# Optimization experiments

Hardware: AMD Instinct MI355X
Metric: run time of the kernel (lower is better)

The kernel has to match this reference:

```python
import jax, jax.numpy as jnp
import numpy as np

IN_F, OUT_F = 4096, 11008
B, S = 2, 4096


def setup_inputs() -> dict:
    key = jax.random.key(0)
    k1, k2, k3, k4 = jax.random.split(key, 4)
    x = jax.random.normal(k1, (B, S, IN_F), dtype=jnp.float32) * 3.0  # pre-smoothed activations
    # int8 weight, stored as int8 (spec'd int32 for harness; math identical)
    weight = jax.random.randint(k2, (OUT_F, IN_F), -127, 128, dtype=jnp.int32).astype(jnp.int8)
    bias = jax.random.normal(k3, (OUT_F,), dtype=jnp.float32)
    dequant_scale = jax.random.uniform(k4, (1,), dtype=jnp.float32) * 0.01 + 0.001  # weight absmax scale
    return {"x": x, "weight": weight, "bias": bias, "dequant_scale": dequant_scale}


def reference(x, weight, bias, dequant_scale):
    x_shape = x.shape
    x2 = x.reshape(-1, x_shape[-1])  # [T, in]
    # per-token activation quantization: absmax -> scale -> round/clamp to int8
    quant_scale = (jnp.max(jnp.abs(x2), axis=-1, keepdims=True) / 127.0).astype(jnp.float32)  # [T,1]
    x_q = jnp.clip(jnp.round(x2 / quant_scale), -128, 127).astype(jnp.int8)
    out_i32 = jnp.matmul(x_q.astype(jnp.int32), weight.astype(jnp.int32).T)  # [T, out]
    # dequant epilogue + bias (all fp32)
    dscale = dequant_scale.reshape(()) * quant_scale  # [T,1]
    out = dscale * out_i32.astype(jnp.float32) + bias
    return out.reshape(*x_shape[:-1], -1).astype(x.dtype)
```

## Files before the change

kernel.cpp:

```cpp
#include <hip/hip_runtime.h>

#define T_TOKENS 8192
#define IN_F 4096
#define OUT_F 11008

#define BM 256
#define BN 256
#define BK 64
#define NT (IN_F / BK)

typedef __attribute__((ext_vector_type(4))) int v4i;
typedef __attribute__((ext_vector_type(16))) int v16i;

__device__ __forceinline__ void load_lds16(const signed char* g, const signed char* l) {
    __builtin_amdgcn_global_load_lds(
        (const __attribute__((address_space(1))) void*)g,
        (__attribute__((address_space(3))) void*)l, 16, 0, 0);
}

__global__ __launch_bounds__(256) void quant_kernel(
        const float* __restrict__ x, signed char* __restrict__ xq,
        float* __restrict__ qscale) {
    const int row = blockIdx.x;
    const float4* xr = (const float4*)(x + (size_t)row * IN_F);
    float4 v[4];
    float am = 0.f;
#pragma unroll
    for (int i = 0; i < 4; ++i) {
        v[i] = xr[threadIdx.x + i * 256];
        am = fmaxf(am, fmaxf(fmaxf(fabsf(v[i].x), fabsf(v[i].y)),
                             fmaxf(fabsf(v[i].z), fabsf(v[i].w))));
    }
#pragma unroll
    for (int off = 32; off > 0; off >>= 1)
        am = fmaxf(am, __shfl_xor(am, off, 64));
    __shared__ float wmax[4];
    const int wid = threadIdx.x >> 6;
    if ((threadIdx.x & 63) == 0) wmax[wid] = am;
    __syncthreads();
    float amax = fmaxf(fmaxf(wmax[0], wmax[1]), fmaxf(wmax[2], wmax[3]));
    float qs = amax * (1.0f / 127.0f);
    if (qs < 1e-30f) qs = 1e-30f;
    const float inv = 1.0f / qs;
    if (threadIdx.x == 0) qscale[row] = qs;
    int* xqo = (int*)(xq + (size_t)row * IN_F);
#pragma unroll
    for (int i = 0; i < 4; ++i) {
        int q0 = (int)rintf(v[i].x * inv);
        int q1 = (int)rintf(v[i].y * inv);
        int q2 = (int)rintf(v[i].z * inv);
        int q3 = (int)rintf(v[i].w * inv);
        q0 = max(-128, min(127, q0));
        q1 = max(-128, min(127, q1));
        q2 = max(-128, min(127, q2));
        q3 = max(-128, min(127, q3));
        unsigned p = (unsigned)(q0 & 255) | ((unsigned)(q1 & 255) << 8) |
                     ((unsigned)(q2 & 255) << 16) | ((unsigned)(q3 & 255) << 24);
        xqo[threadIdx.x + i * 256] = (int)p;
    }
}

__global__ __launch_bounds__(256) void repack_kernel(
        const int* __restrict__ w32, signed char* __restrict__ w8, int n4) {
    int idx = blockIdx.x * 256 + threadIdx.x;
    const int stride = gridDim.x * 256;
    for (int i = idx; i < n4; i += stride) {
        v4i w = ((const v4i*)w32)[i];
        unsigned p = (unsigned)(w[0] & 255) | ((unsigned)(w[1] & 255) << 8) |
                     ((unsigned)(w[2] & 255) << 16) | ((unsigned)(w[3] & 255) << 24);
        ((int*)w8)[i] = (int)p;
    }
}

__global__ __launch_bounds__(512, 2) void gemm_kernel(
        const signed char* __restrict__ A, const signed char* __restrict__ B,
        const float* __restrict__ qscale, const float* __restrict__ bias,
        const float* __restrict__ dqs, float* __restrict__ out) {
    __shared__ __align__(16) signed char smem[3 * 32768];

    const int tid = threadIdx.x;
    const int wid = tid >> 6;
    const int lane = tid & 63;
    const int wm = wid >> 2;
    const int wn = wid & 3;
    const int l31 = lane & 31;
    const int hi = lane >> 5;

    const int b = (int)blockIdx.x;
    const int xcd = b & 7;
    const int idx = b >> 3;
    const int m0 = (xcd * 4 + (idx & 3)) * BM;
    const int n0 = (idx >> 2) * BN;

    const signed char* gSrc[4];
    int ldsOff[4];
#pragma unroll
    for (int c = 0; c < 4; ++c) {
        const int cc = c & 1;
        const int L = cc * 8192 + tid * 16;
        const int row = L >> 6;
        const int slot = (L >> 4) & 3;
        const int col = ((slot ^ ((row >> 1) & 3)) << 4);
        if (c < 2) {
            gSrc[c] = A + (size_t)(m0 + row) * IN_F + col;
            ldsOff[c] = cc * 8192 + wid * 1024;
        } else {
            gSrc[c] = B + (size_t)(n0 + row) * IN_F + col;
            ldsOff[c] = 16384 + cc * 8192 + wid * 1024;
        }
    }

    int aOff[4][2], bOff[2][2];
#pragma unroll
    for (int im = 0; im < 4; ++im) {
        const int r = wm * 128 + im * 32 + l31;
#pragma unroll
        for (int ks = 0; ks < 2; ++ks) {
            const int slot = ks * 2 + hi;
            aOff[im][ks] = r * 64 + ((slot ^ ((r >> 1) & 3)) << 4);
        }
    }
#pragma unroll
    for (int in = 0; in < 2; ++in) {
        const int r = wn * 64 + in * 32 + l31;
#pragma unroll
        for (int ks = 0; ks < 2; ++ks) {
            const int slot = ks * 2 + hi;
            bOff[in][ks] = 16384 + r * 64 + ((slot ^ ((r >> 1) & 3)) << 4);
        }
    }

    v16i acc[4][2] = {};

    int bb0 = 0, bb1 = 32768, bb2 = 65536;
#pragma unroll
    for (int c = 0; c < 4; ++c) load_lds16(gSrc[c], smem + bb0 + ldsOff[c]);
#pragma unroll
    for (int c = 0; c < 4; ++c) load_lds16(gSrc[c] + BK, smem + bb1 + ldsOff[c]);
    asm volatile("s_waitcnt vmcnt(4)" ::: "memory");
    __builtin_amdgcn_sched_barrier(0);
    __builtin_amdgcn_s_barrier();

    for (int t = 0; t < NT; ++t) {
        const int koff2 = (t + 2) * BK;
        const bool stage = (t + 2 < NT);
        v4i a01[2][2], a23[2][2], b0[2], b1[2];

#pragma unroll
        for (int im = 0; im < 2; ++im)
#pragma unroll
            for (int ks = 0; ks < 2; ++ks)
                a01[im][ks] = *(const v4i*)(smem + bb0 + aOff[im][ks]);
#pragma unroll
        for (int ks = 0; ks < 2; ++ks)
            b0[ks] = *(const v4i*)(smem + bb0 + bOff[0][ks]);
        if (stage) load_lds16(gSrc[0] + koff2, smem + bb2 + ldsOff[0]);
        __builtin_amdgcn_sched_barrier(0);
        __builtin_amdgcn_s_barrier();
        asm volatile("s_waitcnt lgkmcnt(0)" ::: "memory");
        __builtin_amdgcn_sched_barrier(0);
        __builtin_amdgcn_s_setprio(1);
#pragma unroll
        for (int ks = 0; ks < 2; ++ks)
#pragma unroll
            for (int im = 0; im < 2; ++im)
                acc[im][0] = __builtin_amdgcn_mfma_i32_32x32x32_i8(
                    a01[im][ks], b0[ks], acc[im][0], 0, 0, 0);
        __builtin_amdgcn_s_setprio(0);
        __builtin_amdgcn_sched_barrier(0);
        __builtin_amdgcn_s_barrier();

#pragma unroll
        for (int ks = 0; ks < 2; ++ks)
            b1[ks] = *(const v4i*)(smem + bb0 + bOff[1][ks]);
        if (stage) load_lds16(gSrc[1] + koff2, smem + bb2 + ldsOff[1]);
        __builtin_amdgcn_sched_barrier(0);
        __builtin_amdgcn_s_barrier();
        asm volatile("s_waitcnt lgkmcnt(0)" ::: "memory");
        __builtin_amdgcn_sched_barrier(0);
        __builtin_amdgcn_s_setprio(1);
#pragma unroll
        for (int ks = 0; ks < 2; ++ks)
#pragma unroll
            for (int im = 0; im < 2; ++im)
                acc[im][1] = __builtin_amdgcn_mfma_i32_32x32x32_i8(
                    a01[im][ks], b1[ks], acc[im][1], 0, 0, 0);
        __builtin_amdgcn_s_setprio(0);
        __builtin_amdgcn_sched_barrier(0);
        __builtin_amdgcn_s_barrier();

#pragma unroll
        for (int im = 0; im < 2; ++im)
#pragma unroll
            for (int ks = 0; ks < 2; ++ks)
                a23[im][ks] = *(const v4i*)(smem + bb0 + aOff[2 + im][ks]);
        if (stage) load_lds16(gSrc[2] + koff2, smem + bb2 + ldsOff[2]);
        __builtin_amdgcn_sched_barrier(0);
        __builtin_amdgcn_s_barrier();
        asm volatile("s_waitcnt lgkmcnt(0)" ::: "memory");
        __builtin_amdgcn_sched_barrier(0);
        __builtin_amdgcn_s_setprio(1);
#pragma unroll
        for (int ks = 0; ks < 2; ++ks)
#pragma unroll
            for (int im = 0; im < 2; ++im)
                acc[2 + im][1] = __builtin_amdgcn_mfma_i32_32x32x32_i8(
                    a23[im][ks], b1[ks], acc[2 + im][1], 0, 0, 0);
        __builtin_amdgcn_s_setprio(0);
        __builtin_amdgcn_sched_barrier(0);
        __builtin_amdgcn_s_barrier();

        if (stage) load_lds16(gSrc[3] + koff2, smem + bb2 + ldsOff[3]);
        __builtin_amdgcn_sched_barrier(0);
        __builtin_amdgcn_s_barrier();
        __builtin_amdgcn_s_setprio(1);
#pragma unroll
        for (int ks = 0; ks < 2; ++ks)
#pragma unroll
            for (int im = 0; im < 2; ++im)
                acc[2 + im][0] = __builtin_amdgcn_mfma_i32_32x32x32_i8(
                    a23[im][ks], b0[ks], acc[2 + im][0], 0, 0, 0);
        __builtin_amdgcn_s_setprio(0);
        __builtin_amdgcn_sched_barrier(0);
        if (t < NT - 2) {
            asm volatile("s_waitcnt vmcnt(4)" ::: "memory");
        } else {
            asm volatile("s_waitcnt vmcnt(0)" ::: "memory");
        }
        __builtin_amdgcn_sched_barrier(0);
        __builtin_amdgcn_s_barrier();

        const int tmp = bb0; bb0 = bb1; bb1 = bb2; bb2 = tmp;
    }

    const float dq = dqs[0];
#pragma unroll
    for (int im = 0; im < 4; ++im) {
        float qsv[16];
#pragma unroll
        for (int r = 0; r < 16; ++r) {
            const int trow = wm * 128 + im * 32 + (r & 3) + 8 * (r >> 2) + 4 * hi;
            qsv[r] = dq * qscale[m0 + trow];
        }
#pragma unroll
        for (int in = 0; in < 2; ++in) {
            const int col = n0 + wn * 64 + in * 32 + l31;
            const float bv = bias[col];
#pragma unroll
            for (int r = 0; r < 16; ++r) {
                const int trow = wm * 128 + im * 32 + (r & 3) + 8 * (r >> 2) + 4 * hi;
                out[(size_t)(m0 + trow) * OUT_F + col] =
                    qsv[r] * (float)acc[im][in][r] + bv;
            }
        }
    }
}

extern "C" void kernel_launch(void* const* d_in, const int* in_sizes, int n_in,
                              void* d_out, int out_size, void* d_ws, size_t ws_size,
                              hipStream_t stream) {
    const float* x    = (const float*)d_in[0];
    const int*   w32  = (const int*)d_in[1];
    const float* bias = (const float*)d_in[2];
    const float* dqs  = (const float*)d_in[3];
    float* out = (float*)d_out;

    signed char* xq = (signed char*)d_ws;
    float* qscale   = (float*)((char*)d_ws + (size_t)T_TOKENS * IN_F);
    signed char* w8 = (signed char*)((char*)d_ws + (size_t)T_TOKENS * IN_F
                                     + (size_t)T_TOKENS * 4);

    quant_kernel<<<T_TOKENS, 256, 0, stream>>>(x, xq, qscale);
    repack_kernel<<<2048, 256, 0, stream>>>(w32, w8, OUT_F * IN_F / 4);
    dim3 g((T_TOKENS / BM) * (OUT_F / BN));
    gemm_kernel<<<g, 512, 0, stream>>>(xq, w8, qscale, bias, dqs, out);
}
```

Before: 535.5 us.

## Deepen GEMM LDS ring to five stages and fuse quant with weight repack

The GEMM main loop moves from a 3-buffer LDS ring to a 5-buffer ring. It processes two K-tiles per iteration, with prefetch three and four tiles ahead. Each phase now issues full 2x2 MFMA blocks with fewer block barriers, which aims to cut synchronisation stalls and hide global-load latency better. The cost is a larger LDS footprint of 160KB per block, which limits occupancy to one block per CU. Separately, the activation quantization and weight repack kernels are merged into a single launch to save one kernel launch and let the two jobs overlap.

```diff
diff --git a/kernel.cpp b/kernel.cpp
--- a/kernel.cpp
+++ b/kernel.cpp
@@ -8,6 +8,7 @@
 #define BN 256
 #define BK 64
 #define NT (IN_F / BK)
+#define NITER (NT / 2)
 
 typedef __attribute__((ext_vector_type(4))) int v4i;
 typedef __attribute__((ext_vector_type(16))) int v16i;
@@ -18,57 +19,58 @@
         (__attribute__((address_space(3))) void*)l, 16, 0, 0);
 }
 
-__global__ __launch_bounds__(256) void quant_kernel(
+__global__ __launch_bounds__(256) void quant_repack_kernel(
         const float* __restrict__ x, signed char* __restrict__ xq,
-        float* __restrict__ qscale) {
-    const int row = blockIdx.x;
-    const float4* xr = (const float4*)(x + (size_t)row * IN_F);
-    float4 v[4];
-    float am = 0.f;
-#pragma unroll
-    for (int i = 0; i < 4; ++i) {
-        v[i] = xr[threadIdx.x + i * 256];
-        am = fmaxf(am, fmaxf(fmaxf(fabsf(v[i].x), fabsf(v[i].y)),
-                             fmaxf(fabsf(v[i].z), fabsf(v[i].w))));
-    }
-#pragma unroll
-    for (int off = 32; off > 0; off >>= 1)
-        am = fmaxf(am, __shfl_xor(am, off, 64));
-    __shared__ float wmax[4];
-    const int wid = threadIdx.x >> 6;
-    if ((threadIdx.x & 63) == 0) wmax[wid] = am;
-    __syncthreads();
-    float amax = fmaxf(fmaxf(wmax[0], wmax[1]), fmaxf(wmax[2], wmax[3]));
-    float qs = amax * (1.0f / 127.0f);
-    if (qs < 1e-30f) qs = 1e-30f;
-    const float inv = 1.0f / qs;
-    if (threadIdx.x == 0) qscale[row] = qs;
-    int* xqo = (int*)(xq + (size_t)row * IN_F);
-#pragma unroll
-    for (int i = 0; i < 4; ++i) {
-        int q0 = (int)rintf(v[i].x * inv);
-        int q1 = (int)rintf(v[i].y * inv);
-        int q2 = (int)rintf(v[i].z * inv);
-        int q3 = (int)rintf(v[i].w * inv);
-        q0 = max(-128, min(127, q0));
-        q1 = max(-128, min(127, q1));
-        q2 = max(-128, min(127, q2));
-        q3 = max(-128, min(127, q3));
-        unsigned p = (unsigned)(q0 & 255) | ((unsigned)(q1 & 255) << 8) |
-                     ((unsigned)(q2 & 255) << 16) | ((unsigned)(q3 & 255) << 24);
-        xqo[threadIdx.x + i * 256] = (int)p;
-    }
-}
-
-__global__ __launch_bounds__(256) void repack_kernel(
-        const int* __restrict__ w32, signed char* __restrict__ w8, int n4) {
-    int idx = blockIdx.x * 256 + threadIdx.x;
-    const int stride = gridDim.x * 256;
-    for (int i = idx; i < n4; i += stride) {
-        v4i w = ((const v4i*)w32)[i];
-        unsigned p = (unsigned)(w[0] & 255) | ((unsigned)(w[1] & 255) << 8) |
-                     ((unsigned)(w[2] & 255) << 16) | ((unsigned)(w[3] & 255) << 24);
-        ((int*)w8)[i] = (int)p;
+        float* __restrict__ qscale, const int* __restrict__ w32,
+        signed char* __restrict__ w8) {
+    if (blockIdx.x < T_TOKENS) {
+        const int row = blockIdx.x;
+        const float4* xr = (const float4*)(x + (size_t)row * IN_F);
+        float4 v[4];
+        float am = 0.f;
+#pragma unroll
+        for (int i = 0; i < 4; ++i) {
+            v[i] = xr[threadIdx.x + i * 256];
+            am = fmaxf(am, fmaxf(fmaxf(fabsf(v[i].x), fabsf(v[i].y)),
+                                 fmaxf(fabsf(v[i].z), fabsf(v[i].w))));
+        }
+#pragma unroll
+        for (int off = 32; off > 0; off >>= 1)
+            am = fmaxf(am, __shfl_xor(am, off, 64));
+        __shared__ float wmax[4];
+        const int wid = threadIdx.x >> 6;
+        if ((threadIdx.x & 63) == 0) wmax[wid] = am;
+        __syncthreads();
+        float amax = fmaxf(fmaxf(wmax[0], wmax[1]), fmaxf(wmax[2], wmax[3]));
+        float qs = amax * (1.0f / 127.0f);
+        if (qs < 1e-30f) qs = 1e-30f;
+        const float inv = 1.0f / qs;
+        if (threadIdx.x == 0) qscale[row] = qs;
+        int* xqo = (int*)(xq + (size_t)row * IN_F);
+#pragma unroll
+        for (int i = 0; i < 4; ++i) {
+            int q0 = (int)rintf(v[i].x * inv);
+            int q1 = (int)rintf(v[i].y * inv);
+            int q2 = (int)rintf(v[i].z * inv);
+            int q3 = (int)rintf(v[i].w * inv);
+            q0 = max(-128, min(127, q0));
+            q1 = max(-128, min(127, q1));
+            q2 = max(-128, min(127, q2));
+            q3 = max(-128, min(127, q3));
+            unsigned p = (unsigned)(q0 & 255) | ((unsigned)(q1 & 255) << 8) |
+                         ((unsigned)(q2 & 255) << 16) | ((unsigned)(q3 & 255) << 24);
+            xqo[threadIdx.x + i * 256] = (int)p;
+        }
+    } else {
+        const int n4 = OUT_F * IN_F / 4;
+        int idx = (blockIdx.x - T_TOKENS) * 256 + threadIdx.x;
+        const int stride = 2048 * 256;
+        for (int i = idx; i < n4; i += stride) {
+            v4i w = ((const v4i*)w32)[i];
+            unsigned p = (unsigned)(w[0] & 255) | ((unsigned)(w[1] & 255) << 8) |
+                         ((unsigned)(w[2] & 255) << 16) | ((unsigned)(w[3] & 255) << 24);
+            ((int*)w8)[i] = (int)p;
+        }
     }
 }
 
@@ -76,7 +78,7 @@
         const signed char* __restrict__ A, const signed char* __restrict__ B,
         const float* __restrict__ qscale, const float* __restrict__ bias,
         const float* __restrict__ dqs, float* __restrict__ out) {
-    __shared__ __align__(16) signed char smem[3 * 32768];
+    __shared__ __align__(16) signed char smem[5 * 32768];
 
     const int tid = threadIdx.x;
     const int wid = tid >> 6;
@@ -132,29 +134,68 @@
 
     v16i acc[4][2] = {};
 
-    int bb0 = 0, bb1 = 32768, bb2 = 65536;
-#pragma unroll
-    for (int c = 0; c < 4; ++c) load_lds16(gSrc[c], smem + bb0 + ldsOff[c]);
-#pragma unroll
-    for (int c = 0; c < 4; ++c) load_lds16(gSrc[c] + BK, smem + bb1 + ldsOff[c]);
+#pragma unroll
+    for (int tt = 0; tt < 3; ++tt)
+#pragma unroll
+        for (int c = 0; c < 4; ++c)
+            load_lds16(gSrc[c] + tt * BK, smem + tt * 32768 + ldsOff[c]);
     asm volatile("s_waitcnt vmcnt(4)" ::: "memory");
     __builtin_amdgcn_sched_barrier(0);
     __builtin_amdgcn_s_barrier();
 
-    for (int t = 0; t < NT; ++t) {
-        const int koff2 = (t + 2) * BK;
-        const bool stage = (t + 2 < NT);
-        v4i a01[2][2], a23[2][2], b0[2], b1[2];
+    int bx = 0;
+    for (int i = 0; i < NITER; ++i) {
+        const int t0 = 2 * i;
+        const int by = (bx + 1 >= 5) ? bx - 4 : bx + 1;
+        const int z3 = (bx + 3 >= 5) ? bx - 2 : bx + 3;
+        const int z4 = (bx + 4 >= 5) ? bx - 1 : bx + 4;
+        const signed char* s0 = smem + bx * 32768;
+        const signed char* s1 = smem + by * 32768;
+        const bool stA = (t0 + 3 < NT);
+        const bool stB = (t0 + 4 < NT);
+        const int k3 = (t0 + 3) * BK;
+        const int k4 = (t0 + 4) * BK;
+
+        v4i a[2][2], bf[2][2];
 
 #pragma unroll
         for (int im = 0; im < 2; ++im)
 #pragma unroll
             for (int ks = 0; ks < 2; ++ks)
-                a01[im][ks] = *(const v4i*)(smem + bb0 + aOff[im][ks]);
+                a[im][ks] = *(const v4i*)(s0 + aOff[im][ks]);
+#pragma unroll
+        for (int in = 0; in < 2; ++in)
+#pragma unroll
+            for (int ks = 0; ks < 2; ++ks)
+                bf[in][ks] = *(const v4i*)(s0 + bOff[in][ks]);
+        if (stA) {
+            load_lds16(gSrc[0] + k3, smem + z3 * 32768 + ldsOff[0]);
+            load_lds16(gSrc[1] + k3, smem + z3 * 32768 + ldsOff[1]);
+        }
+        __builtin_amdgcn_sched_barrier(0);
+        __builtin_amdgcn_s_barrier();
+        asm volatile("s_waitcnt lgkmcnt(0)" ::: "memory");
+        __builtin_amdgcn_sched_barrier(0);
+        __builtin_amdgcn_s_setprio(1);
 #pragma unroll
         for (int ks = 0; ks < 2; ++ks)
-            b0[ks] = *(const v4i*)(smem + bb0 + bOff[0][ks]);
-        if (stage) load_lds16(gSrc[0] + koff2, smem + bb2 + ldsOff[0]);
+#pragma unroll
+            for (int im = 0; im < 2; ++im)
+#pragma unroll
+                for (int in = 0; in < 2; ++in)
+                    acc[im][in] = __builtin_amdgcn_mfma_i32_32x32x32_i8(
+                        a[im][ks], bf[in][ks], acc[im][in], 0, 0, 0);
+        __builtin_amdgcn_s_setprio(0);
+
+#pragma unroll
+        for (int im = 0; im < 2; ++im)
+#pragma unroll
+            for (int ks = 0; ks < 2; ++ks)
+                a[im][ks] = *(const v4i*)(s0 + aOff[2 + im][ks]);
+        if (stA) {
+            load_lds16(gSrc[2] + k3, smem + z3 * 32768 + ldsOff[2]);
+            load_lds16(gSrc[3] + k3, smem + z3 * 32768 + ldsOff[3]);
+        }
         __builtin_amdgcn_sched_barrier(0);
         __builtin_amdgcn_s_barrier();
         asm volatile("s_waitcnt lgkmcnt(0)" ::: "memory");
@@ -164,16 +205,50 @@
         for (int ks = 0; ks < 2; ++ks)
 #pragma unroll
             for (int im = 0; im < 2; ++im)
-                acc[im][0] = __builtin_amdgcn_mfma_i32_32x32x32_i8(
-                    a01[im][ks], b0[ks], acc[im][0], 0, 0, 0);
+#pragma unroll
+                for (int in = 0; in < 2; ++in)
+                    acc[2 + im][in] = __builtin_amdgcn_mfma_i32_32x32x32_i8(
+                        a[im][ks], bf[in][ks], acc[2 + im][in], 0, 0, 0);
         __builtin_amdgcn_s_setprio(0);
-        __builtin_amdgcn_sched_barrier(0);
-        __builtin_amdgcn_s_barrier();
-
+
+#pragma unroll
+        for (int im = 0; im < 2; ++im)
+#pragma unroll
+            for (int ks = 0; ks < 2; ++ks)
+                a[im][ks] = *(const v4i*)(s1 + aOff[im][ks]);
+#pragma unroll
+        for (int in = 0; in < 2; ++in)
+#pragma unroll
+            for (int ks = 0; ks < 2; ++ks)
+                bf[in][ks] = *(const v4i*)(s1 + bOff[in][ks]);
+        if (stB) {
+            load_lds16(gSrc[0] + k4, smem + z4 * 32768 + ldsOff[0]);
+            load_lds16(gSrc[1] + k4, smem + z4 * 32768 + ldsOff[1]);
+        }
+        __builtin_amdgcn_sched_barrier(0);
+        __builtin_amdgcn_s_barrier();
+        asm volatile("s_waitcnt lgkmcnt(0)" ::: "memory");
+        __builtin_amdgcn_sched_barrier(0);
+        __builtin_amdgcn_s_setprio(1);
 #pragma unroll
         for (int ks = 0; ks < 2; ++ks)
-            b1[ks] = *(const v4i*)(smem + bb0 + bOff[1][ks]);
-        if (stage) load_lds16(gSrc[1] + koff2, smem + bb2 + ldsOff[1]);
+#pragma unroll
+            for (int im = 0; im < 2; ++im)
+#pragma unroll
+                for (int in = 0; in < 2; ++in)
+                    acc[im][in] = __builtin_amdgcn_mfma_i32_32x32x32_i8(
+                        a[im][ks], bf[in][ks], acc[im][in], 0, 0, 0);
+        __builtin_amdgcn_s_setprio(0);
+
+#pragma unroll
+        for (int im = 0; im < 2; ++im)
+#pragma unroll
+            for (int ks = 0; ks < 2; ++ks)
+                a[im][ks] = *(const v4i*)(s1 + aOff[2 + im][ks]);
+        if (stB) {
+            load_lds16(gSrc[2] + k4, smem + z4 * 32768 + ldsOff[2]);
+            load_lds16(gSrc[3] + k4, smem + z4 * 32768 + ldsOff[3]);
+        }
         __builtin_amdgcn_sched_barrier(0);
         __builtin_amdgcn_s_barrier();
         asm volatile("s_waitcnt lgkmcnt(0)" ::: "memory");
@@ -183,46 +258,14 @@
         for (int ks = 0; ks < 2; ++ks)
 #pragma unroll
             for (int im = 0; im < 2; ++im)
-                acc[im][1] = __builtin_amdgcn_mfma_i32_32x32x32_i8(
-                    a01[im][ks], b1[ks], acc[im][1], 0, 0, 0);
+#pragma unroll
+                for (int in = 0; in < 2; ++in)
+                    acc[2 + im][in] = __builtin_amdgcn_mfma_i32_32x32x32_i8(
+                        a[im][ks], bf[in][ks], acc[2 + im][in], 0, 0, 0);
         __builtin_amdgcn_s_setprio(0);
-        __builtin_amdgcn_sched_barrier(0);
-        __builtin_amdgcn_s_barrier();
-
-#pragma unroll
-        for (int im = 0; im < 2; ++im)
-#pragma unroll
-            for (int ks = 0; ks < 2; ++ks)
-                a23[im][ks] = *(const v4i*)(smem + bb0 + aOff[2 + im][ks]);
-        if (stage) load_lds16(gSrc[2] + koff2, smem + bb2 + ldsOff[2]);
-        __builtin_amdgcn_sched_barrier(0);
-        __builtin_amdgcn_s_barrier();
-        asm volatile("s_waitcnt lgkmcnt(0)" ::: "memory");
-        __builtin_amdgcn_sched_barrier(0);
-        __builtin_amdgcn_s_setprio(1);
-#pragma unroll
-        for (int ks = 0; ks < 2; ++ks)
-#pragma unroll
-            for (int im = 0; im < 2; ++im)
-                acc[2 + im][1] = __builtin_amdgcn_mfma_i32_32x32x32_i8(
-                    a23[im][ks], b1[ks], acc[2 + im][1], 0, 0, 0);
-        __builtin_amdgcn_s_setprio(0);
-        __builtin_amdgcn_sched_barrier(0);
-        __builtin_amdgcn_s_barrier();
-
-        if (stage) load_lds16(gSrc[3] + koff2, smem + bb2 + ldsOff[3]);
-        __builtin_amdgcn_sched_barrier(0);
-        __builtin_amdgcn_s_barrier();
-        __builtin_amdgcn_s_setprio(1);
-#pragma unroll
-        for (int ks = 0; ks < 2; ++ks)
-#pragma unroll
-            for (int im = 0; im < 2; ++im)
-                acc[2 + im][0] = __builtin_amdgcn_mfma_i32_32x32x32_i8(
-                    a23[im][ks], b0[ks], acc[2 + im][0], 0, 0, 0);
-        __builtin_amdgcn_s_setprio(0);
-        __builtin_amdgcn_sched_barrier(0);
-        if (t < NT - 2) {
+
+        __builtin_amdgcn_sched_barrier(0);
+        if (stB) {
             asm volatile("s_waitcnt vmcnt(4)" ::: "memory");
         } else {
             asm volatile("s_waitcnt vmcnt(0)" ::: "memory");
@@ -230,7 +273,7 @@
         __builtin_amdgcn_sched_barrier(0);
         __builtin_amdgcn_s_barrier();
 
-        const int tmp = bb0; bb0 = bb1; bb1 = bb2; bb2 = tmp;
+        bx = (bx + 2 >= 5) ? bx - 3 : bx + 2;
     }
 
     const float dq = dqs[0];
@@ -270,8 +313,7 @@
     signed char* w8 = (signed char*)((char*)d_ws + (size_t)T_TOKENS * IN_F
                                      + (size_t)T_TOKENS * 4);
 
-    quant_kernel<<<T_TOKENS, 256, 0, stream>>>(x, xq, qscale);
-    repack_kernel<<<2048, 256, 0, stream>>>(w32, w8, OUT_F * IN_F / 4);
+    quant_repack_kernel<<<T_TOKENS + 2048, 256, 0, stream>>>(x, xq, qscale, w32, w8);
     dim3 g((T_TOKENS / BM) * (OUT_F / BN));
     gemm_kernel<<<g, 512, 0, stream>>>(xq, w8, qscale, bias, dqs, out);
 }
```

Measured after the change: 508.0 us. -5.1%, faster.
